# Performance work log

Hardware: AMD Instinct MI355X
Metric: run time of the kernel (lower is better)

## Reference

```python
import jax, jax.numpy as jnp
import numpy as np
import math
from jax import lax

N = 5          # kernel_size (hard-coded PHT assumes 5x5)
K = N // 2     # 2
EPS = 1e-6
THETA = 0.7

def _pht_kernel_np():
    # H_i = cos(2*pi*2*r^2 + 0*theta) on the 5x5 grid, times calibrated spectral weights, plus eps
    coords = np.arange(N, dtype=np.float32) - K
    gv, gu = np.meshgrid(coords, coords, indexing='ij')  # torch.meshgrid default is 'ij'
    r2 = (gu ** 2 + gv ** 2) / (K * K + EPS)
    H = np.cos(2.0 * math.pi * 2.0 * r2).astype(np.float32)
    target = np.zeros((N, N), np.float32)
    target[K, K] = -4.0
    target[K - 1, K] = 1.0
    target[K + 1, K] = 1.0
    target[K, K - 1] = 1.0
    target[K, K + 1] = 1.0
    sw = np.where(target != 0, target / H, 0.0).astype(np.float32)
    return (H * sw + EPS).astype(np.float32)  # (5,5)

def _rotation_maps_np():
    # Replicates rotate_kernel exactly: float32 cos/sin, int() truncation, later (h,w) overwrite.
    angles = np.linspace(0, 2 * np.pi, 8, endpoint=False)
    SH = np.zeros((8, N, N), np.int32)
    SW = np.zeros((8, N, N), np.int32)
    M = np.zeros((8, N, N), np.float32)
    for ai, a in enumerate(angles):
        c = float(np.cos(np.float32(a)))
        s = float(np.sin(np.float32(a)))
        for h in range(N):
            for w in range(N):
                rh = int(h * c + w * (-s))
                rw = int(h * s + w * c)
                if 0 <= rh < N and 0 <= rw < N:
                    SH[ai, rh, rw] = h
                    SW[ai, rh, rw] = w
                    M[ai, rh, rw] = 1.0
    return SH, SW, M

_PHT = jnp.asarray(_pht_kernel_np())                     # (5,5)
_sh, _sw, _m = _rotation_maps_np()
_SH = jnp.asarray(_sh)
_SW = jnp.asarray(_sw)
_MASK = jnp.asarray(_m)

def setup_inputs() -> dict:
    key = jax.random.key(0)
    k1, k2 = jax.random.split(key)
    x = jax.random.normal(k1, (32, 64, 128, 128), dtype=jnp.float32)
    weight = jax.random.normal(k2, (64, 64, 5, 5), dtype=jnp.float32) * 0.05
    alpha = jnp.ones((1,), dtype=jnp.float32)
    return {"x": x, "weight": weight, "alpha": alpha}

def reference(x, weight, alpha):
    # Branch 1: PHT-modulated weight, averaged over 8 SO(2) rotations.
    # pht_kernel is (C_in,1,5,5) with identical values per channel -> broadcast (5,5).
    w_eff = weight * alpha[0] * _PHT[None, None]          # (Co,Ci,5,5)
    # rotated[o,i,a,rh,rw] = w_eff[o,i,SH[a,rh,rw],SW[a,rh,rw]] * MASK
    rotated = w_eff[:, :, _SH, _SW] * _MASK               # (Co,Ci,8,5,5)
    # conv is linear in weight: mean of 8 convs == conv with mean kernel
    mean_k = rotated.mean(axis=2)                         # (Co,Ci,5,5)
    out = lax.conv_general_dilated(
        x, mean_k, window_strides=(1, 1), padding=[(2, 2), (2, 2)],
        dimension_numbers=("NCHW", "OIHW", "NCHW"))
    # Branch 2: 1x1 kernel_diff; rotation of a 1x1 kernel is identity, mean of 8 == single conv.
    kd = weight.sum(axis=(2, 3))                          # (Co,Ci)
    out_diff = jnp.einsum("oi,bihw->bohw", kd, x)
    return out - THETA * out_diff
```

## Files before the change

kernel.cpp:

```cpp
#include <hip/hip_runtime.h>
#include <stdint.h>

typedef __attribute__((ext_vector_type(8))) __bf16 bf16x8;
typedef __attribute__((ext_vector_type(16))) float f32x16;
typedef __attribute__((ext_vector_type(4))) unsigned int u32x4;
typedef __attribute__((ext_vector_type(2))) unsigned int u32x2;
typedef __attribute__((ext_vector_type(4))) float f32x4;
typedef __attribute__((ext_vector_type(2))) float f32x2;
typedef unsigned int u32;
typedef unsigned short u16;

#define THETA 0.7f

__host__ __device__ constexpr float pht_val(int q) {
  return (q == 12) ? (-4.0f + 1e-6f)
       : (q == 7 || q == 11 || q == 13 || q == 17) ? (1.0f + 1e-6f)
       : 1e-6f;
}

__device__ __forceinline__ u16 f2bf(float v) {
  u32 u = __builtin_bit_cast(u32, v);
  return (u16)((u + 0x7fffu + ((u >> 16) & 1u)) >> 16);
}

__global__ __launch_bounds__(256) void k_prep(const float* __restrict__ wgt,
                                              const float* __restrict__ alpha,
                                              u16* __restrict__ apack) {
  int t = blockIdx.x * 256 + threadIdx.x;
  int o = t >> 6, ci = t & 63;
  const float* wp = wgt + ((size_t)(o * 64 + ci)) * 25;
  float wv[25], sumw = 0.f;
#pragma unroll
  for (int p = 0; p < 25; ++p) { wv[p] = wp[p]; sumw += wv[p]; }
  float keff[25];
#pragma unroll
  for (int p = 0; p < 25; ++p) keff[p] = pht_val(p) * wv[p];
  constexpr int TP[33] = {0,1,2,3,4,6,7,9,12,13,  0,1,2,3,4,  0, 0, 0,
                          0,5,10,15,20,  0,5,6,10,11,12,15,17,20,21};
  constexpr int TQ[33] = {5,6,12,17,23,10,16,22,20,21,  0,5,10,15,20,  5, 0, 5,
                          0,6,7,8,9,  5,6,2,12,8,4,17,9,23,14};
#pragma unroll
  for (int e = 0; e < 33; ++e) keff[TP[e]] += pht_val(TQ[e]) * wv[TQ[e]];

  float al = alpha[0];
  int kc = ci >> 4, oh = o >> 5;
  int lane = ((ci >> 3) & 1) * 32 + (o & 31);
#pragma unroll
  for (int p = 0; p < 25; ++p) {
    float v = al * (keff[p] * 0.125f);
    if (p == 12) v -= THETA * sumw;
    size_t idx = ((((size_t)p * 4 + kc) * 2 + oh) * 64 + lane) * 8 + (ci & 7);
    apack[idx] = f2bf(v);
  }
}

#define GSTR 1168
#define RSTR 2336
#define BUFSZ 18688

#define MM(A, B, C) __builtin_amdgcn_mfma_f32_32x32x16_bf16((A), __builtin_bit_cast(bf16x8, (B)), (C), 0, 0, 0)

#define PK2(A_, B_) ({ u32 r_;                                              \
    asm("v_cvt_pk_bf16_f32 %0, %1, %2" : "=v"(r_) : "v"(A_), "v"(B_));      \
    r_; })

#define LDBR(DX, KC) do {                                                   \
    const char* pb_ = tile + (((KC) & 1) * BUFSZ) + rbase + (DX) * 16;      \
    br0 = *(const u32x4*)(pb_ + 0 * RSTR);                                  \
    br1 = *(const u32x4*)(pb_ + 1 * RSTR);                                  \
    br2 = *(const u32x4*)(pb_ + 2 * RSTR);                                  \
    br3 = *(const u32x4*)(pb_ + 3 * RSTR);                                  \
    br4 = *(const u32x4*)(pb_ + 4 * RSTR);                                  \
    br5 = *(const u32x4*)(pb_ + 5 * RSTR);                                  \
  } while (0)

#define LDAF(DX, KC) do {                                                   \
    af0 = apb[(size_t)((0 * 5 + (DX)) * 512 + (KC) * 128)];                 \
    af1 = apb[(size_t)((1 * 5 + (DX)) * 512 + (KC) * 128)];                 \
    af2 = apb[(size_t)((2 * 5 + (DX)) * 512 + (KC) * 128)];                 \
    af3 = apb[(size_t)((3 * 5 + (DX)) * 512 + (KC) * 128)];                 \
    af4 = apb[(size_t)((4 * 5 + (DX)) * 512 + (KC) * 128)];                 \
  } while (0)

#define BURST() do {                                                        \
    bf16x8 A_;                                                              \
    A_ = __builtin_bit_cast(bf16x8, af0);                                   \
    a0 = MM(A_, br0, a0); a1 = MM(A_, br1, a1);                             \
    A_ = __builtin_bit_cast(bf16x8, af1);                                   \
    a0 = MM(A_, br1, a0); a1 = MM(A_, br2, a1);                             \
    A_ = __builtin_bit_cast(bf16x8, af2);                                   \
    a0 = MM(A_, br2, a0); a1 = MM(A_, br3, a1);                             \
    A_ = __builtin_bit_cast(bf16x8, af3);                                   \
    a0 = MM(A_, br3, a0); a1 = MM(A_, br4, a1);                             \
    A_ = __builtin_bit_cast(bf16x8, af4);                                   \
    a0 = MM(A_, br4, a0); a1 = MM(A_, br5, a1);                             \
  } while (0)

#define DXITER(DX, KC) do { LDBR(DX, KC); LDAF(DX, KC); BURST(); } while (0)

#define TBAR() do {                                                         \
    asm volatile("s_waitcnt lgkmcnt(0)" ::: "memory");                      \
    __builtin_amdgcn_sched_barrier(0);                                      \
    __builtin_amdgcn_s_barrier();                                           \
    __builtin_amdgcn_sched_barrier(0);                                      \
  } while (0)

#define SLOADP(P) do {                                                      \
    if (rowok) {                                                            \
      const float* pm_ = xrow + (size_t)(16 * (P) + 8 * gp + 4 * hh) * 16384 + pxm; \
      sm0 = *(const f32x4*)(pm_);                                           \
      sm1 = *(const f32x4*)(pm_ + 16384);                                   \
      sm2 = *(const f32x4*)(pm_ + 2 * 16384);                               \
      sm3 = *(const f32x4*)(pm_ + 3 * 16384);                               \
    } else { sm0 = 0; sm1 = 0; sm2 = 0; sm3 = 0; }                          \
    if (hdut) {                                                             \
      if (hok) {                                                            \
        const float* ph_ = xn + (size_t)hsy * 128                           \
                           + (size_t)(16 * (P) + 8 * hgp + 4 * hhh) * 16384 + hpx; \
        sh0 = *(const f32x2*)(ph_);                                         \
        sh1 = *(const f32x2*)(ph_ + 16384);                                 \
        sh2 = *(const f32x2*)(ph_ + 2 * 16384);                             \
        sh3 = *(const f32x2*)(ph_ + 3 * 16384);                             \
      } else { sh0 = 0; sh1 = 0; sh2 = 0; sh3 = 0; }                        \
    }                                                                       \
  } while (0)

#define SWRITEP(P) do {                                                     \
    char* wb_ = tile + (((P) & 1) * BUFSZ) + rr * RSTR + gp * GSTR + hh * 8;\
    u32x2 w_;                                                               \
    w_[0] = PK2(sm0.x, sm1.x); w_[1] = PK2(sm2.x, sm3.x);                   \
    *(u32x2*)(wb_ + (cbm + 0) * 16) = w_;                                   \
    w_[0] = PK2(sm0.y, sm1.y); w_[1] = PK2(sm2.y, sm3.y);                   \
    *(u32x2*)(wb_ + (cbm + 1) * 16) = w_;                                   \
    w_[0] = PK2(sm0.z, sm1.z); w_[1] = PK2(sm2.z, sm3.z);                   \
    *(u32x2*)(wb_ + (cbm + 2) * 16) = w_;                                   \
    w_[0] = PK2(sm0.w, sm1.w); w_[1] = PK2(sm2.w, sm3.w);                   \
    *(u32x2*)(wb_ + (cbm + 3) * 16) = w_;                                   \
    if (hdut) {                                                             \
      char* hb_ = tile + (((P) & 1) * BUFSZ) + hrr * RSTR + hgp * GSTR + hhh * 8; \
      u32x2 u_;                                                             \
      u_[0] = PK2(sh0.x, sh1.x); u_[1] = PK2(sh2.x, sh3.x);                 \
      *(u32x2*)(hb_ + (hc + 0) * 16) = u_;                                  \
      u_[0] = PK2(sh0.y, sh1.y); u_[1] = PK2(sh2.y, sh3.y);                 \
      *(u32x2*)(hb_ + (hc + 1) * 16) = u_;                                  \
    }                                                                       \
  } while (0)

#define CPHASE(SP, CP) do {                                                 \
    SLOADP(SP);                                                             \
    DXITER(0, CP);                                                          \
    DXITER(1, CP);                                                          \
    DXITER(2, CP);                                                          \
    DXITER(3, CP);                                                          \
    SWRITEP(SP);                                                            \
    DXITER(4, CP);                                                          \
    TBAR();                                                                 \
  } while (0)

__global__ __launch_bounds__(512, 4) void k_conv(const float* __restrict__ x,
                                                 const u32x4* __restrict__ apv,
                                                 float* __restrict__ out) {
  __shared__ char tile[2 * BUFSZ];
  int bid = blockIdx.x;
  int lg = (bid & 7) * 256 + (bid >> 3);
  int ph = lg & 1, yt = (lg >> 1) & 31, n = lg >> 6;
  int y0 = yt * 4, px0 = ph * 64;
  int tid = threadIdx.x;
  int l = tid & 63;

  const float* xn = x + (size_t)n * (64 * 16384);
  int rr = tid >> 6;
  int qq = (tid >> 2) & 15, gp = (tid >> 1) & 1, hh = tid & 1;
  int sy = y0 + rr - 2;
  bool rowok = (unsigned)sy < 128u;
  const float* xrow = xn + (size_t)(rowok ? sy : 0) * 128;
  int pxm = px0 + 4 * qq;
  int cbm = 4 + 4 * qq;
  bool hdut = tid < 64;
  int hrr = tid >> 3, hside = (tid >> 2) & 1, hgp = (tid >> 1) & 1, hhh = tid & 1;
  int hpx = hside ? px0 + 64 : px0 - 2;
  int hc = hside ? 68 : 2;
  int hsy = y0 + hrr - 2;
  bool hok = ((unsigned)hpx < 127u) && ((unsigned)hsy < 128u);
  if (!hok) hsy = 0; if (hpx < 0) hpx = 0;

  int wv = tid >> 6;
  int oh = wv >> 2, q32 = (wv >> 1) & 1, rp = wv & 1;
  int l31 = l & 31, lhi = l >> 5;
  const u32x4* apb = apv + (size_t)(oh * 64 + l);
  int rbase = 2 * rp * RSTR + lhi * GSTR + (q32 * 32 + l31 + 2) * 16;

  f32x4 sm0, sm1, sm2, sm3;
  f32x2 sh0, sh1, sh2, sh3;
  u32x4 br0, br1, br2, br3, br4, br5;
  u32x4 af0, af1, af2, af3, af4;
  f32x16 a0 = 0, a1 = 0;

  SLOADP(0);
  SWRITEP(0);
  TBAR();
  CPHASE(1, 0);
  CPHASE(2, 1);
  CPHASE(3, 2);
  DXITER(0, 3);
  DXITER(1, 3);
  DXITER(2, 3);
  DXITER(3, 3);
  DXITER(4, 3);

  float* ob = out + ((size_t)(n * 64 + oh * 32) * 128 + (y0 + 2 * rp)) * 128
              + px0 + q32 * 32 + l31;
#pragma unroll
  for (int rg = 0; rg < 16; ++rg) {
    int orow = (rg & 3) + 8 * (rg >> 2) + 4 * lhi;
    float* obr = ob + (size_t)orow * 16384;
    obr[0]   = a0[rg];
    obr[128] = a1[rg];
  }
}

extern "C" void kernel_launch(void* const* d_in, const int* in_sizes, int n_in,
                              void* d_out, int out_size, void* d_ws, size_t ws_size,
                              hipStream_t stream) {
  const float* x     = (const float*)d_in[0];
  const float* wgt   = (const float*)d_in[1];
  const float* alpha = (const float*)d_in[2];
  float* out = (float*)d_out;

  u16* apack = (u16*)d_ws;

  k_prep<<<16,   256, 0, stream>>>(wgt, alpha, apack);
  k_conv<<<2048, 512, 0, stream>>>(x, (const u32x4*)apack, out);
}
```

Measured before the change: 138.1 us.

## Give each wave a private LDS input tile and drop block barriers

The conv kernel moves from 512-thread blocks sharing one LDS tile (with s_barrier per channel phase) to 256-thread blocks where each wave stages its own 6-row input slab and computes both 32-channel output halves. This removes cross-wave barriers and doubles A-fragment reuse per B load, at the cost of redundant halo loads between waves, more registers (four accumulators, eight staging vectors) and lower occupancy bounds.

Result: slower. 159.6 us (+15.5%).

```diff
diff --git a/kernel.cpp b/kernel.cpp
--- a/kernel.cpp
+++ b/kernel.cpp
@@ -4,7 +4,6 @@
 typedef __attribute__((ext_vector_type(8))) __bf16 bf16x8;
 typedef __attribute__((ext_vector_type(16))) float f32x16;
 typedef __attribute__((ext_vector_type(4))) unsigned int u32x4;
-typedef __attribute__((ext_vector_type(2))) unsigned int u32x2;
 typedef __attribute__((ext_vector_type(4))) float f32x4;
 typedef __attribute__((ext_vector_type(2))) float f32x2;
 typedef unsigned int u32;
@@ -54,9 +53,11 @@
   }
 }
 
-#define GSTR 1168
-#define RSTR 2336
-#define BUFSZ 18688
+#define RS 1312
+#define SS 656
+#define BUFB 7872
+#define WVB 15744
+#define PSTEP 262144
 
 #define MM(A, B, C) __builtin_amdgcn_mfma_f32_32x32x16_bf16((A), __builtin_bit_cast(bf16x8, (B)), (C), 0, 0, 0)
 
@@ -65,157 +66,234 @@
     r_; })
 
 #define LDBR(DX, KC) do {                                                   \
-    const char* pb_ = tile + (((KC) & 1) * BUFSZ) + rbase + (DX) * 16;      \
-    br0 = *(const u32x4*)(pb_ + 0 * RSTR);                                  \
-    br1 = *(const u32x4*)(pb_ + 1 * RSTR);                                  \
-    br2 = *(const u32x4*)(pb_ + 2 * RSTR);                                  \
-    br3 = *(const u32x4*)(pb_ + 3 * RSTR);                                  \
-    br4 = *(const u32x4*)(pb_ + 4 * RSTR);                                  \
-    br5 = *(const u32x4*)(pb_ + 5 * RSTR);                                  \
+    const char* pb_ = rdb + (((KC) & 1) * BUFB) + (DX) * 16;                \
+    br0 = *(const u32x4*)(pb_ + 0 * RS);                                    \
+    br1 = *(const u32x4*)(pb_ + 1 * RS);                                    \
+    br2 = *(const u32x4*)(pb_ + 2 * RS);                                    \
+    br3 = *(const u32x4*)(pb_ + 3 * RS);                                    \
+    br4 = *(const u32x4*)(pb_ + 4 * RS);                                    \
+    br5 = *(const u32x4*)(pb_ + 5 * RS);                                    \
   } while (0)
 
 #define LDAF(DX, KC) do {                                                   \
-    af0 = apb[(size_t)((0 * 5 + (DX)) * 512 + (KC) * 128)];                 \
-    af1 = apb[(size_t)((1 * 5 + (DX)) * 512 + (KC) * 128)];                 \
-    af2 = apb[(size_t)((2 * 5 + (DX)) * 512 + (KC) * 128)];                 \
-    af3 = apb[(size_t)((3 * 5 + (DX)) * 512 + (KC) * 128)];                 \
-    af4 = apb[(size_t)((4 * 5 + (DX)) * 512 + (KC) * 128)];                 \
+    af00 = apb[(size_t)((0 * 5 + (DX)) * 512 + (KC) * 128)];                \
+    af01 = apb[(size_t)((1 * 5 + (DX)) * 512 + (KC) * 128)];                \
+    af02 = apb[(size_t)((2 * 5 + (DX)) * 512 + (KC) * 128)];                \
+    af03 = apb[(size_t)((3 * 5 + (DX)) * 512 + (KC) * 128)];                \
+    af04 = apb[(size_t)((4 * 5 + (DX)) * 512 + (KC) * 128)];                \
+    af10 = apb[(size_t)((0 * 5 + (DX)) * 512 + (KC) * 128 + 64)];           \
+    af11 = apb[(size_t)((1 * 5 + (DX)) * 512 + (KC) * 128 + 64)];           \
+    af12 = apb[(size_t)((2 * 5 + (DX)) * 512 + (KC) * 128 + 64)];           \
+    af13 = apb[(size_t)((3 * 5 + (DX)) * 512 + (KC) * 128 + 64)];           \
+    af14 = apb[(size_t)((4 * 5 + (DX)) * 512 + (KC) * 128 + 64)];           \
   } while (0)
 
 #define BURST() do {                                                        \
     bf16x8 A_;                                                              \
-    A_ = __builtin_bit_cast(bf16x8, af0);                                   \
-    a0 = MM(A_, br0, a0); a1 = MM(A_, br1, a1);                             \
-    A_ = __builtin_bit_cast(bf16x8, af1);                                   \
-    a0 = MM(A_, br1, a0); a1 = MM(A_, br2, a1);                             \
-    A_ = __builtin_bit_cast(bf16x8, af2);                                   \
-    a0 = MM(A_, br2, a0); a1 = MM(A_, br3, a1);                             \
-    A_ = __builtin_bit_cast(bf16x8, af3);                                   \
-    a0 = MM(A_, br3, a0); a1 = MM(A_, br4, a1);                             \
-    A_ = __builtin_bit_cast(bf16x8, af4);                                   \
-    a0 = MM(A_, br4, a0); a1 = MM(A_, br5, a1);                             \
-  } while (0)
-
-#define DXITER(DX, KC) do { LDBR(DX, KC); LDAF(DX, KC); BURST(); } while (0)
-
-#define TBAR() do {                                                         \
+    A_ = __builtin_bit_cast(bf16x8, af00);                                  \
+    a00 = MM(A_, br0, a00); a10 = MM(A_, br1, a10);                         \
+    A_ = __builtin_bit_cast(bf16x8, af10);                                  \
+    a01 = MM(A_, br0, a01); a11 = MM(A_, br1, a11);                         \
+    A_ = __builtin_bit_cast(bf16x8, af01);                                  \
+    a00 = MM(A_, br1, a00); a10 = MM(A_, br2, a10);                         \
+    A_ = __builtin_bit_cast(bf16x8, af11);                                  \
+    a01 = MM(A_, br1, a01); a11 = MM(A_, br2, a11);                         \
+    A_ = __builtin_bit_cast(bf16x8, af02);                                  \
+    a00 = MM(A_, br2, a00); a10 = MM(A_, br3, a10);                         \
+    A_ = __builtin_bit_cast(bf16x8, af12);                                  \
+    a01 = MM(A_, br2, a01); a11 = MM(A_, br3, a11);                         \
+    A_ = __builtin_bit_cast(bf16x8, af03);                                  \
+    a00 = MM(A_, br3, a00); a10 = MM(A_, br4, a10);                         \
+    A_ = __builtin_bit_cast(bf16x8, af13);                                  \
+    a01 = MM(A_, br3, a01); a11 = MM(A_, br4, a11);                         \
+    A_ = __builtin_bit_cast(bf16x8, af04);                                  \
+    a00 = MM(A_, br4, a00); a10 = MM(A_, br5, a10);                         \
+    A_ = __builtin_bit_cast(bf16x8, af14);                                  \
+    a01 = MM(A_, br4, a01); a11 = MM(A_, br5, a11);                         \
+  } while (0)
+
+#define DXI(DX, KC) do { LDBR(DX, KC); LDAF(DX, KC); BURST(); } while (0)
+
+#define SLOADA(P) do {                                                      \
+    if (okA) {                                                              \
+      const float* p_ = pA + (size_t)(P) * PSTEP;                           \
+      smA0 = *(const f32x4*)(p_);              smA1 = *(const f32x4*)(p_ + 16384);      \
+      smA2 = *(const f32x4*)(p_ + 2 * 16384);  smA3 = *(const f32x4*)(p_ + 3 * 16384);  \
+      smA4 = *(const f32x4*)(p_ + 4 * 16384);  smA5 = *(const f32x4*)(p_ + 5 * 16384);  \
+      smA6 = *(const f32x4*)(p_ + 6 * 16384);  smA7 = *(const f32x4*)(p_ + 7 * 16384);  \
+    } else {                                                                \
+      smA0 = 0; smA1 = 0; smA2 = 0; smA3 = 0;                               \
+      smA4 = 0; smA5 = 0; smA6 = 0; smA7 = 0;                               \
+    }                                                                       \
+  } while (0)
+
+#define SWRITEA(P) do {                                                     \
+    char* w_ = wA + (((P) & 1) * BUFB);                                     \
+    u32x4 t_;                                                               \
+    t_[0] = PK2(smA0.x, smA1.x); t_[1] = PK2(smA2.x, smA3.x);               \
+    t_[2] = PK2(smA4.x, smA5.x); t_[3] = PK2(smA6.x, smA7.x);               \
+    *(u32x4*)(w_ + 0)  = t_;                                                \
+    t_[0] = PK2(smA0.y, smA1.y); t_[1] = PK2(smA2.y, smA3.y);               \
+    t_[2] = PK2(smA4.y, smA5.y); t_[3] = PK2(smA6.y, smA7.y);               \
+    *(u32x4*)(w_ + 16) = t_;                                                \
+    t_[0] = PK2(smA0.z, smA1.z); t_[1] = PK2(smA2.z, smA3.z);               \
+    t_[2] = PK2(smA4.z, smA5.z); t_[3] = PK2(smA6.z, smA7.z);               \
+    *(u32x4*)(w_ + 32) = t_;                                                \
+    t_[0] = PK2(smA0.w, smA1.w); t_[1] = PK2(smA2.w, smA3.w);               \
+    t_[2] = PK2(smA4.w, smA5.w); t_[3] = PK2(smA6.w, smA7.w);               \
+    *(u32x4*)(w_ + 48) = t_;                                                \
+  } while (0)
+
+#define SLOADB(P) do {                                                      \
+    if (okB) {                                                              \
+      const float* p_ = pB + (size_t)(P) * PSTEP;                           \
+      smA0 = *(const f32x4*)(p_);              smA1 = *(const f32x4*)(p_ + 16384);      \
+      smA2 = *(const f32x4*)(p_ + 2 * 16384);  smA3 = *(const f32x4*)(p_ + 3 * 16384);  \
+      smA4 = *(const f32x4*)(p_ + 4 * 16384);  smA5 = *(const f32x4*)(p_ + 5 * 16384);  \
+      smA6 = *(const f32x4*)(p_ + 6 * 16384);  smA7 = *(const f32x4*)(p_ + 7 * 16384);  \
+    } else {                                                                \
+      smA0 = 0; smA1 = 0; smA2 = 0; smA3 = 0;                               \
+      smA4 = 0; smA5 = 0; smA6 = 0; smA7 = 0;                               \
+    }                                                                       \
+  } while (0)
+
+#define SWRITEB(P) do {                                                     \
+    if (mB) {                                                               \
+      char* w_ = wB + (((P) & 1) * BUFB);                                   \
+      u32x4 t_;                                                             \
+      t_[0] = PK2(smA0.x, smA1.x); t_[1] = PK2(smA2.x, smA3.x);             \
+      t_[2] = PK2(smA4.x, smA5.x); t_[3] = PK2(smA6.x, smA7.x);             \
+      *(u32x4*)(w_ + 0)  = t_;                                              \
+      t_[0] = PK2(smA0.y, smA1.y); t_[1] = PK2(smA2.y, smA3.y);             \
+      t_[2] = PK2(smA4.y, smA5.y); t_[3] = PK2(smA6.y, smA7.y);             \
+      *(u32x4*)(w_ + 16) = t_;                                              \
+      t_[0] = PK2(smA0.z, smA1.z); t_[1] = PK2(smA2.z, smA3.z);             \
+      t_[2] = PK2(smA4.z, smA5.z); t_[3] = PK2(smA6.z, smA7.z);             \
+      *(u32x4*)(w_ + 32) = t_;                                              \
+      t_[0] = PK2(smA0.w, smA1.w); t_[1] = PK2(smA2.w, smA3.w);             \
+      t_[2] = PK2(smA4.w, smA5.w); t_[3] = PK2(smA6.w, smA7.w);             \
+      *(u32x4*)(w_ + 48) = t_;                                              \
+    }                                                                       \
+  } while (0)
+
+#define SLOADH(P) do {                                                      \
+    if (okH) {                                                              \
+      const float* p_ = pH + (size_t)(P) * PSTEP;                           \
+      shH0 = *(const f32x2*)(p_);              shH1 = *(const f32x2*)(p_ + 16384);      \
+      shH2 = *(const f32x2*)(p_ + 2 * 16384);  shH3 = *(const f32x2*)(p_ + 3 * 16384);  \
+      shH4 = *(const f32x2*)(p_ + 4 * 16384);  shH5 = *(const f32x2*)(p_ + 5 * 16384);  \
+      shH6 = *(const f32x2*)(p_ + 6 * 16384);  shH7 = *(const f32x2*)(p_ + 7 * 16384);  \
+    } else {                                                                \
+      shH0 = 0; shH1 = 0; shH2 = 0; shH3 = 0;                               \
+      shH4 = 0; shH5 = 0; shH6 = 0; shH7 = 0;                               \
+    }                                                                       \
+  } while (0)
+
+#define SWRITEH(P) do {                                                     \
+    if (mH) {                                                               \
+      char* w_ = wH + (((P) & 1) * BUFB);                                   \
+      u32x4 t_;                                                             \
+      t_[0] = PK2(shH0.x, shH1.x); t_[1] = PK2(shH2.x, shH3.x);             \
+      t_[2] = PK2(shH4.x, shH5.x); t_[3] = PK2(shH6.x, shH7.x);             \
+      *(u32x4*)(w_ + 0)  = t_;                                              \
+      t_[0] = PK2(shH0.y, shH1.y); t_[1] = PK2(shH2.y, shH3.y);             \
+      t_[2] = PK2(shH4.y, shH5.y); t_[3] = PK2(shH6.y, shH7.y);             \
+      *(u32x4*)(w_ + 16) = t_;                                              \
+    }                                                                       \
+  } while (0)
+
+#define SBAR0() __builtin_amdgcn_sched_barrier(0)
+
+#define CPHASE(P, KC) do {                                                  \
+    SLOADA(P);                                                              \
+    DXI(0, KC);                                                             \
+    DXI(1, KC);                                                             \
+    SWRITEA(P); SBAR0();                                                    \
+    SLOADB(P);                                                              \
+    DXI(2, KC);                                                             \
+    SWRITEB(P); SBAR0();                                                    \
+    SLOADH(P);                                                              \
+    DXI(3, KC);                                                             \
+    SWRITEH(P);                                                             \
+    DXI(4, KC);                                                             \
     asm volatile("s_waitcnt lgkmcnt(0)" ::: "memory");                      \
-    __builtin_amdgcn_sched_barrier(0);                                      \
-    __builtin_amdgcn_s_barrier();                                           \
-    __builtin_amdgcn_sched_barrier(0);                                      \
-  } while (0)
-
-#define SLOADP(P) do {                                                      \
-    if (rowok) {                                                            \
-      const float* pm_ = xrow + (size_t)(16 * (P) + 8 * gp + 4 * hh) * 16384 + pxm; \
-      sm0 = *(const f32x4*)(pm_);                                           \
-      sm1 = *(const f32x4*)(pm_ + 16384);                                   \
-      sm2 = *(const f32x4*)(pm_ + 2 * 16384);                               \
-      sm3 = *(const f32x4*)(pm_ + 3 * 16384);                               \
-    } else { sm0 = 0; sm1 = 0; sm2 = 0; sm3 = 0; }                          \
-    if (hdut) {                                                             \
-      if (hok) {                                                            \
-        const float* ph_ = xn + (size_t)hsy * 128                           \
-                           + (size_t)(16 * (P) + 8 * hgp + 4 * hhh) * 16384 + hpx; \
-        sh0 = *(const f32x2*)(ph_);                                         \
-        sh1 = *(const f32x2*)(ph_ + 16384);                                 \
-        sh2 = *(const f32x2*)(ph_ + 2 * 16384);                             \
-        sh3 = *(const f32x2*)(ph_ + 3 * 16384);                             \
-      } else { sh0 = 0; sh1 = 0; sh2 = 0; sh3 = 0; }                        \
-    }                                                                       \
-  } while (0)
-
-#define SWRITEP(P) do {                                                     \
-    char* wb_ = tile + (((P) & 1) * BUFSZ) + rr * RSTR + gp * GSTR + hh * 8;\
-    u32x2 w_;                                                               \
-    w_[0] = PK2(sm0.x, sm1.x); w_[1] = PK2(sm2.x, sm3.x);                   \
-    *(u32x2*)(wb_ + (cbm + 0) * 16) = w_;                                   \
-    w_[0] = PK2(sm0.y, sm1.y); w_[1] = PK2(sm2.y, sm3.y);                   \
-    *(u32x2*)(wb_ + (cbm + 1) * 16) = w_;                                   \
-    w_[0] = PK2(sm0.z, sm1.z); w_[1] = PK2(sm2.z, sm3.z);                   \
-    *(u32x2*)(wb_ + (cbm + 2) * 16) = w_;                                   \
-    w_[0] = PK2(sm0.w, sm1.w); w_[1] = PK2(sm2.w, sm3.w);                   \
-    *(u32x2*)(wb_ + (cbm + 3) * 16) = w_;                                   \
-    if (hdut) {                                                             \
-      char* hb_ = tile + (((P) & 1) * BUFSZ) + hrr * RSTR + hgp * GSTR + hhh * 8; \
-      u32x2 u_;                                                             \
-      u_[0] = PK2(sh0.x, sh1.x); u_[1] = PK2(sh2.x, sh3.x);                 \
-      *(u32x2*)(hb_ + (hc + 0) * 16) = u_;                                  \
-      u_[0] = PK2(sh0.y, sh1.y); u_[1] = PK2(sh2.y, sh3.y);                 \
-      *(u32x2*)(hb_ + (hc + 1) * 16) = u_;                                  \
-    }                                                                       \
-  } while (0)
-
-#define CPHASE(SP, CP) do {                                                 \
-    SLOADP(SP);                                                             \
-    DXITER(0, CP);                                                          \
-    DXITER(1, CP);                                                          \
-    DXITER(2, CP);                                                          \
-    DXITER(3, CP);                                                          \
-    SWRITEP(SP);                                                            \
-    DXITER(4, CP);                                                          \
-    TBAR();                                                                 \
-  } while (0)
-
-__global__ __launch_bounds__(512, 4) void k_conv(const float* __restrict__ x,
+    SBAR0();                                                                \
+  } while (0)
+
+__global__ __launch_bounds__(256, 2) void k_conv(const float* __restrict__ x,
                                                  const u32x4* __restrict__ apv,
                                                  float* __restrict__ out) {
-  __shared__ char tile[2 * BUFSZ];
+  __shared__ char tile[4 * WVB];
   int bid = blockIdx.x;
   int lg = (bid & 7) * 256 + (bid >> 3);
   int ph = lg & 1, yt = (lg >> 1) & 31, n = lg >> 6;
   int y0 = yt * 4, px0 = ph * 64;
   int tid = threadIdx.x;
-  int l = tid & 63;
+  int l = tid & 63, wv = tid >> 6;
+  int q32 = wv >> 1, rp = wv & 1;
+  int pxq = px0 + q32 * 32;
+  int yA = y0 + 2 * rp;
+  int l31 = l & 31, lhi = l >> 5;
 
   const float* xn = x + (size_t)n * (64 * 16384);
-  int rr = tid >> 6;
-  int qq = (tid >> 2) & 15, gp = (tid >> 1) & 1, hh = tid & 1;
-  int sy = y0 + rr - 2;
-  bool rowok = (unsigned)sy < 128u;
-  const float* xrow = xn + (size_t)(rowok ? sy : 0) * 128;
-  int pxm = px0 + 4 * qq;
-  int cbm = 4 + 4 * qq;
-  bool hdut = tid < 64;
-  int hrr = tid >> 3, hside = (tid >> 2) & 1, hgp = (tid >> 1) & 1, hhh = tid & 1;
-  int hpx = hside ? px0 + 64 : px0 - 2;
-  int hc = hside ? 68 : 2;
-  int hsy = y0 + hrr - 2;
-  bool hok = ((unsigned)hpx < 127u) && ((unsigned)hsy < 128u);
-  if (!hok) hsy = 0; if (hpx < 0) hpx = 0;
-
-  int wv = tid >> 6;
-  int oh = wv >> 2, q32 = (wv >> 1) & 1, rp = wv & 1;
-  int l31 = l & 31, lhi = l >> 5;
-  const u32x4* apb = apv + (size_t)(oh * 64 + l);
-  int rbase = 2 * rp * RSTR + lhi * GSTR + (q32 * 32 + l31 + 2) * 16;
-
-  f32x4 sm0, sm1, sm2, sm3;
-  f32x2 sh0, sh1, sh2, sh3;
+  char* wbase = tile + wv * WVB;
+
+  int jA = l >> 4, sgA = (l >> 3) & 1, qiA = l & 7;
+  int syA = yA - 2 + jA;
+  bool okA = (unsigned)syA < 128u;
+  const float* pA = xn + (size_t)(8 * sgA) * 16384
+                    + (size_t)(okA ? syA : 0) * 128 + pxq + 4 * qiA;
+  char* wA = wbase + jA * RS + sgA * SS + (4 + 4 * qiA) * 16;
+  bool mB = l < 32;
+  int jB = 4 + (l >> 4), sgB = (l >> 3) & 1, qiB = l & 7;
+  int syB = yA - 2 + jB;
+  bool okB = mB && (unsigned)syB < 128u;
+  const float* pB = xn + (size_t)(8 * sgB) * 16384
+                    + (size_t)(okB ? syB : 0) * 128 + pxq + 4 * qiB;
+  char* wB = wbase + (mB ? jB : 0) * RS + sgB * SS + (4 + 4 * qiB) * 16;
+  bool mH = l < 24;
+  int jH = l >> 2, sgH = (l >> 1) & 1, sdH = l & 1;
+  int syH = yA - 2 + jH;
+  int pxH = sdH ? pxq + 32 : pxq - 2;
+  bool okH = mH && ((unsigned)syH < 128u) && ((unsigned)pxH < 127u);
+  const float* pH = xn + (size_t)(8 * sgH) * 16384
+                    + (size_t)(okH ? syH : 0) * 128 + (okH ? pxH : 0);
+  char* wH = wbase + (mH ? jH : 0) * RS + sgH * SS + (sdH ? 36 : 2) * 16;
+
+  const u32x4* apb = apv + l;
+  const char* rdb = wbase + lhi * SS + (l31 + 2) * 16;
+
+  f32x4 smA0, smA1, smA2, smA3, smA4, smA5, smA6, smA7;
+  f32x2 shH0, shH1, shH2, shH3, shH4, shH5, shH6, shH7;
   u32x4 br0, br1, br2, br3, br4, br5;
-  u32x4 af0, af1, af2, af3, af4;
-  f32x16 a0 = 0, a1 = 0;
-
-  SLOADP(0);
-  SWRITEP(0);
-  TBAR();
+  u32x4 af00, af01, af02, af03, af04, af10, af11, af12, af13, af14;
+  f32x16 a00 = 0, a01 = 0, a10 = 0, a11 = 0;
+
+  SLOADA(0); SWRITEA(0); SBAR0();
+  SLOADB(0); SWRITEB(0); SBAR0();
+  SLOADH(0); SWRITEH(0);
+  asm volatile("s_waitcnt lgkmcnt(0)" ::: "memory");
+  SBAR0();
+
   CPHASE(1, 0);
   CPHASE(2, 1);
   CPHASE(3, 2);
-  DXITER(0, 3);
-  DXITER(1, 3);
-  DXITER(2, 3);
-  DXITER(3, 3);
-  DXITER(4, 3);
-
-  float* ob = out + ((size_t)(n * 64 + oh * 32) * 128 + (y0 + 2 * rp)) * 128
-              + px0 + q32 * 32 + l31;
+  DXI(0, 3);
+  DXI(1, 3);
+  DXI(2, 3);
+  DXI(3, 3);
+  DXI(4, 3);
+
+  float* ob = out + ((size_t)(n * 64) * 128 + yA) * 128 + pxq + l31;
 #pragma unroll
   for (int rg = 0; rg < 16; ++rg) {
-    int orow = (rg & 3) + 8 * (rg >> 2) + 4 * lhi;
-    float* obr = ob + (size_t)orow * 16384;
-    obr[0]   = a0[rg];
-    obr[128] = a1[rg];
+    int rowc = (rg & 3) + 8 * (rg >> 2) + 4 * lhi;
+    float* o0 = ob + (size_t)rowc * 16384;
+    float* o1 = o0 + (size_t)32 * 16384;
+    o0[0]   = a00[rg];
+    o0[128] = a10[rg];
+    o1[0]   = a01[rg];
+    o1[128] = a11[rg];
   }
 }
 
@@ -230,5 +308,5 @@
   u16* apack = (u16*)d_ws;
 
   k_prep<<<16,   256, 0, stream>>>(wgt, alpha, apack);
-  k_conv<<<2048, 512, 0, stream>>>(x, (const u32x4*)apack, out);
-}
+  k_conv<<<2048, 256, 0, stream>>>(x, (const u32x4*)apack, out);
+}
```
